# Kernel optimization log

Measured on AMD Instinct MI355X. Metric: run time of the kernel, lower is better.

The kernel has to match this reference:

```python
import jax, jax.numpy as jnp
import numpy as np

DIM = 64
OUT_DIM = 32
ALPHA = 16
BRANCH = 4
DEPTH = 7  # levels 0..DEPTH; level l has BRANCH**l nodes
SIZES = [BRANCH ** l for l in range(DEPTH + 1)]
OFFS = np.cumsum([0] + SIZES).tolist()  # OFFS[l] = start index of level l (BFS order)
N = OFFS[-1]  # 21845


def _build_children():
    # complete 4-ary tree in BFS order; leaves get 0 (never read)
    ch = np.zeros((N, BRANCH), dtype=np.int32)
    for l in range(DEPTH):
        off, size = OFFS[l], SIZES[l]
        base = OFFS[l + 1] + BRANCH * np.arange(size)
        ch[off:off + size] = base[:, None] + np.arange(BRANCH)[None, :]
    return jnp.asarray(ch)


def setup_inputs() -> dict:
    key = jax.random.key(0)
    k1, k2, k3, k4, k5 = jax.random.split(key, 5)
    sym = jax.random.randint(k1, (N,), 0, ALPHA, dtype=jnp.int32)
    children = _build_children()
    s = 1.0 / np.sqrt(DIM)
    W = jax.random.normal(k2, (ALPHA, DIM, DIM), dtype=jnp.float32) * s      # per-symbol Linear weight [out,in]
    b = jax.random.normal(k3, (ALPHA, DIM), dtype=jnp.float32) * s           # per-symbol Linear bias
    W_out = jax.random.normal(k4, (OUT_DIM, DIM), dtype=jnp.float32) * s
    b_out = jax.random.normal(k5, (OUT_DIM,), dtype=jnp.float32) * s
    return {"sym": sym, "children": children, "W": W, "b": b,
            "W_out": W_out, "b_out": b_out}


def _forward(W, b, W_out, b_out, sym, children):
    enc = jnp.zeros((N, DIM), dtype=W.dtype)
    # process levels bottom-up (children before parents) -- batches the
    # original node-by-node stack recursion by tree depth
    for l in range(DEPTH, -1, -1):
        off, size = OFFS[l], SIZES[l]
        syms = sym[off:off + size]                      # [size]
        if l == DEPTH:
            # leaves: layer applied to zero vector
            h = jnp.zeros((size, DIM), dtype=W.dtype)
        else:
            ch = children[off:off + size]               # [size, 4]
            h = enc[ch].mean(axis=1)                    # gather children encodings + mean
        Wn = W[syms]                                    # [size, dim, dim] symbol-routed weights
        bn = b[syms]                                    # [size, dim]
        e = jax.nn.sigmoid(jnp.einsum('nij,nj->ni', Wn, h) + bn)
        enc = enc.at[off:off + size].set(e)
    # root is node 0 in BFS order
    return enc[0] @ W_out.T + b_out                     # [OUT_DIM]


def reference(sym, children, W, b, W_out, b_out):
    return _forward(W, b, W_out, b_out, sym, children)
```

## Files before the change

### kernel.cpp

```cpp
#include <hip/hip_runtime.h>

#define DIM 64


__device__ __forceinline__ float sigmoidf_(float x) {
    return 1.0f / (1.0f + __expf(-x));
}

__device__ __forceinline__ float matvec_sig(const float* __restrict__ W,
                                            const float* __restrict__ B,
                                            int s, int lane,
                                            const float* h) {
    const float4* wrow = reinterpret_cast<const float4*>(W + (size_t)s * DIM * DIM + lane * DIM);
    const float4* h4   = reinterpret_cast<const float4*>(h);
    float acc = B[s * DIM + lane];
#pragma unroll
    for (int j = 0; j < DIM / 4; ++j) {
        float4 wv = wrow[j];
        float4 hv = h4[j];
        acc = fmaf(wv.x, hv.x, acc);
        acc = fmaf(wv.y, hv.y, acc);
        acc = fmaf(wv.z, hv.z, acc);
        acc = fmaf(wv.w, hv.w, acc);
    }
    return sigmoidf_(acc);
}

__global__ __launch_bounds__(256) void k_lvl654(const int* __restrict__ sym,
                                                const float* __restrict__ W,
                                                const float* __restrict__ B,
                                                float* __restrict__ enc4) {
    __shared__ __align__(16) float h6[16][DIM];
    __shared__ __align__(16) float e6[16][DIM];
    __shared__ __align__(16) float hb[4][DIM];
    __shared__ __align__(16) float e5[4][DIM];
    const int tid  = threadIdx.x;
    const int lane = tid & 63;
    const int wv   = tid >> 6;
    const int b    = blockIdx.x;

#pragma unroll
    for (int it = 0; it < 4; ++it) {
        int q = it * 4 + wv;
        int leaf0 = 5461 + b * 64 + q * 4;
        float acc = 0.0f;
#pragma unroll
        for (int c = 0; c < 4; ++c) {
            int s = sym[leaf0 + c];
            acc += sigmoidf_(B[s * DIM + lane]);
        }
        h6[q][lane] = 0.25f * acc;
    }
    __syncthreads();
#pragma unroll
    for (int it = 0; it < 4; ++it) {
        int q = it * 4 + wv;
        int p = 1365 + b * 16 + q;
        e6[q][lane] = matvec_sig(W, B, sym[p], lane, &h6[q][0]);
    }
    __syncthreads();
    hb[wv][lane] = 0.25f * (e6[4 * wv + 0][lane] + e6[4 * wv + 1][lane] +
                            e6[4 * wv + 2][lane] + e6[4 * wv + 3][lane]);
    __syncthreads();
    {
        int m = 341 + b * 4 + wv;
        e5[wv][lane] = matvec_sig(W, B, sym[m], lane, &hb[wv][0]);
    }
    __syncthreads();
    if (wv == 0) {
        hb[0][lane] = 0.25f * (e5[0][lane] + e5[1][lane] + e5[2][lane] + e5[3][lane]);
    }
    __syncthreads();
    if (wv == 0) {
        int n = 85 + b;
        enc4[b * DIM + lane] = matvec_sig(W, B, sym[n], lane, &hb[0][0]);
    }
}

__global__ __launch_bounds__(256) void k_lvl32(const int* __restrict__ sym,
                                               const float* __restrict__ W,
                                               const float* __restrict__ B,
                                               const float* __restrict__ enc4,
                                               float* __restrict__ enc2) {
    __shared__ __align__(16) float h3[4][DIM];
    __shared__ __align__(16) float e3[4][DIM];
    __shared__ __align__(16) float hb[DIM];
    const int tid  = threadIdx.x;
    const int lane = tid & 63;
    const int wv   = tid >> 6;
    const int b    = blockIdx.x;

    {
        int c0 = 16 * b + 4 * wv;
        float acc = enc4[(c0 + 0) * DIM + lane] + enc4[(c0 + 1) * DIM + lane] +
                    enc4[(c0 + 2) * DIM + lane] + enc4[(c0 + 3) * DIM + lane];
        h3[wv][lane] = 0.25f * acc;
    }
    __syncthreads();
    {
        int n = 21 + 4 * b + wv;
        e3[wv][lane] = matvec_sig(W, B, sym[n], lane, &h3[wv][0]);
    }
    __syncthreads();
    if (wv == 0) {
        hb[lane] = 0.25f * (e3[0][lane] + e3[1][lane] + e3[2][lane] + e3[3][lane]);
    }
    __syncthreads();
    if (wv == 0) {
        int n = 5 + b;
        enc2[b * DIM + lane] = matvec_sig(W, B, sym[n], lane, hb);
    }
}

__global__ __launch_bounds__(256) void k_lvl10_out(const int* __restrict__ sym,
                                                   const float* __restrict__ W,
                                                   const float* __restrict__ B,
                                                   const float* __restrict__ Wout,
                                                   const float* __restrict__ bout,
                                                   const float* __restrict__ enc2,
                                                   float* __restrict__ out) {
    __shared__ __align__(16) float h1[4][DIM];
    __shared__ __align__(16) float e1[4][DIM];
    __shared__ __align__(16) float hb[DIM];
    __shared__ __align__(16) float e0[DIM];
    const int tid  = threadIdx.x;
    const int lane = tid & 63;
    const int wv   = tid >> 6;

    {
        int c0 = 4 * wv;
        float acc = enc2[(c0 + 0) * DIM + lane] + enc2[(c0 + 1) * DIM + lane] +
                    enc2[(c0 + 2) * DIM + lane] + enc2[(c0 + 3) * DIM + lane];
        h1[wv][lane] = 0.25f * acc;
    }
    __syncthreads();
    {
        int m = 1 + wv;
        e1[wv][lane] = matvec_sig(W, B, sym[m], lane, &h1[wv][0]);
    }
    __syncthreads();
    if (wv == 0) {
        hb[lane] = 0.25f * (e1[0][lane] + e1[1][lane] + e1[2][lane] + e1[3][lane]);
    }
    __syncthreads();
    if (wv == 0) {
        e0[lane] = matvec_sig(W, B, sym[0], lane, hb);
    }
    __syncthreads();
    if (tid < 32) {
        const float4* wrow = reinterpret_cast<const float4*>(Wout + tid * DIM);
        const float4* h4   = reinterpret_cast<const float4*>(e0);
        float acc = bout[tid];
#pragma unroll
        for (int j = 0; j < DIM / 4; ++j) {
            float4 w = wrow[j];
            float4 h = h4[j];
            acc = fmaf(w.x, h.x, acc);
            acc = fmaf(w.y, h.y, acc);
            acc = fmaf(w.z, h.z, acc);
            acc = fmaf(w.w, h.w, acc);
        }
        out[tid] = acc;
    }
}

extern "C" void kernel_launch(void* const* d_in, const int* in_sizes, int n_in,
                              void* d_out, int out_size, void* d_ws, size_t ws_size,
                              hipStream_t stream) {
    const int*   sym  = (const int*)d_in[0];
    const float* W    = (const float*)d_in[2];
    const float* B    = (const float*)d_in[3];
    const float* Wout = (const float*)d_in[4];
    const float* bout = (const float*)d_in[5];
    float* out  = (float*)d_out;
    float* enc4 = (float*)d_ws;
    float* enc2 = enc4 + 256 * DIM;

    k_lvl654<<<256, 256, 0, stream>>>(sym, W, B, enc4);
    k_lvl32 <<<16,  256, 0, stream>>>(sym, W, B, enc4, enc2);
    k_lvl10_out<<<1, 256, 0, stream>>>(sym, W, B, Wout, bout, enc2, out);
}
```

Before: 83.53 us.

## Fuse three level kernels into one cooperative kernel with grid sync

```diff
diff --git a/kernel.cpp b/kernel.cpp
--- a/kernel.cpp
+++ b/kernel.cpp
@@ -1,4 +1,7 @@
 #include <hip/hip_runtime.h>
+#include <hip/hip_cooperative_groups.h>
+
+namespace cg = cooperative_groups;
 
 #define DIM 64
 
@@ -26,141 +29,109 @@
     return sigmoidf_(acc);
 }
 
-__global__ __launch_bounds__(256) void k_lvl654(const int* __restrict__ sym,
-                                                const float* __restrict__ W,
-                                                const float* __restrict__ B,
-                                                float* __restrict__ enc4) {
+__global__ __launch_bounds__(1024) void recnet_all(const int* __restrict__ sym,
+                                                   const float* __restrict__ W,
+                                                   const float* __restrict__ B,
+                                                   const float* __restrict__ Wout,
+                                                   const float* __restrict__ bout,
+                                                   float* __restrict__ enc4,
+                                                   float* __restrict__ out) {
     __shared__ __align__(16) float h6[16][DIM];
     __shared__ __align__(16) float e6[16][DIM];
+    __shared__ __align__(16) float e5[4][DIM];
     __shared__ __align__(16) float hb[4][DIM];
-    __shared__ __align__(16) float e5[4][DIM];
+    __shared__ __align__(16) float e3[64][DIM];
+    __shared__ __align__(16) float e2[16][DIM];
+
     const int tid  = threadIdx.x;
     const int lane = tid & 63;
-    const int wv   = tid >> 6;
+    const int w    = tid >> 6;
     const int b    = blockIdx.x;
 
-#pragma unroll
-    for (int it = 0; it < 4; ++it) {
-        int q = it * 4 + wv;
-        int leaf0 = 5461 + b * 64 + q * 4;
+    {
+        int leaf0 = 5461 + b * 64 + w * 4;
         float acc = 0.0f;
 #pragma unroll
         for (int c = 0; c < 4; ++c) {
             int s = sym[leaf0 + c];
             acc += sigmoidf_(B[s * DIM + lane]);
         }
-        h6[q][lane] = 0.25f * acc;
+        h6[w][lane] = 0.25f * acc;
     }
     __syncthreads();
-#pragma unroll
-    for (int it = 0; it < 4; ++it) {
-        int q = it * 4 + wv;
-        int p = 1365 + b * 16 + q;
-        e6[q][lane] = matvec_sig(W, B, sym[p], lane, &h6[q][0]);
+    {
+        int p = 1365 + b * 16 + w;
+        e6[w][lane] = matvec_sig(W, B, sym[p], lane, &h6[w][0]);
     }
     __syncthreads();
-    hb[wv][lane] = 0.25f * (e6[4 * wv + 0][lane] + e6[4 * wv + 1][lane] +
-                            e6[4 * wv + 2][lane] + e6[4 * wv + 3][lane]);
-    __syncthreads();
-    {
-        int m = 341 + b * 4 + wv;
-        e5[wv][lane] = matvec_sig(W, B, sym[m], lane, &hb[wv][0]);
+    if (w < 4) {
+        hb[w][lane] = 0.25f * (e6[4 * w + 0][lane] + e6[4 * w + 1][lane] +
+                               e6[4 * w + 2][lane] + e6[4 * w + 3][lane]);
     }
     __syncthreads();
-    if (wv == 0) {
+    if (w < 4) {
+        int m = 341 + b * 4 + w;
+        e5[w][lane] = matvec_sig(W, B, sym[m], lane, &hb[w][0]);
+    }
+    __syncthreads();
+    if (w == 0) {
         hb[0][lane] = 0.25f * (e5[0][lane] + e5[1][lane] + e5[2][lane] + e5[3][lane]);
     }
     __syncthreads();
-    if (wv == 0) {
-        int n = 85 + b;
-        enc4[b * DIM + lane] = matvec_sig(W, B, sym[n], lane, &hb[0][0]);
+    if (w == 0) {
+        enc4[b * DIM + lane] = matvec_sig(W, B, sym[85 + b], lane, &hb[0][0]);
     }
-}
 
-__global__ __launch_bounds__(256) void k_lvl32(const int* __restrict__ sym,
-                                               const float* __restrict__ W,
-                                               const float* __restrict__ B,
-                                               const float* __restrict__ enc4,
-                                               float* __restrict__ enc2) {
-    __shared__ __align__(16) float h3[4][DIM];
-    __shared__ __align__(16) float e3[4][DIM];
-    __shared__ __align__(16) float hb[DIM];
-    const int tid  = threadIdx.x;
-    const int lane = tid & 63;
-    const int wv   = tid >> 6;
-    const int b    = blockIdx.x;
+    cg::this_grid().sync();
 
-    {
-        int c0 = 16 * b + 4 * wv;
-        float acc = enc4[(c0 + 0) * DIM + lane] + enc4[(c0 + 1) * DIM + lane] +
-                    enc4[(c0 + 2) * DIM + lane] + enc4[(c0 + 3) * DIM + lane];
-        h3[wv][lane] = 0.25f * acc;
-    }
-    __syncthreads();
-    {
-        int n = 21 + 4 * b + wv;
-        e3[wv][lane] = matvec_sig(W, B, sym[n], lane, &h3[wv][0]);
-    }
-    __syncthreads();
-    if (wv == 0) {
-        hb[lane] = 0.25f * (e3[0][lane] + e3[1][lane] + e3[2][lane] + e3[3][lane]);
-    }
-    __syncthreads();
-    if (wv == 0) {
-        int n = 5 + b;
-        enc2[b * DIM + lane] = matvec_sig(W, B, sym[n], lane, hb);
-    }
-}
-
-__global__ __launch_bounds__(256) void k_lvl10_out(const int* __restrict__ sym,
-                                                   const float* __restrict__ W,
-                                                   const float* __restrict__ B,
-                                                   const float* __restrict__ Wout,
-                                                   const float* __restrict__ bout,
-                                                   const float* __restrict__ enc2,
-                                                   float* __restrict__ out) {
-    __shared__ __align__(16) float h1[4][DIM];
-    __shared__ __align__(16) float e1[4][DIM];
-    __shared__ __align__(16) float hb[DIM];
-    __shared__ __align__(16) float e0[DIM];
-    const int tid  = threadIdx.x;
-    const int lane = tid & 63;
-    const int wv   = tid >> 6;
-
-    {
-        int c0 = 4 * wv;
-        float acc = enc2[(c0 + 0) * DIM + lane] + enc2[(c0 + 1) * DIM + lane] +
-                    enc2[(c0 + 2) * DIM + lane] + enc2[(c0 + 3) * DIM + lane];
-        h1[wv][lane] = 0.25f * acc;
-    }
-    __syncthreads();
-    {
-        int m = 1 + wv;
-        e1[wv][lane] = matvec_sig(W, B, sym[m], lane, &h1[wv][0]);
-    }
-    __syncthreads();
-    if (wv == 0) {
-        hb[lane] = 0.25f * (e1[0][lane] + e1[1][lane] + e1[2][lane] + e1[3][lane]);
-    }
-    __syncthreads();
-    if (wv == 0) {
-        e0[lane] = matvec_sig(W, B, sym[0], lane, hb);
-    }
-    __syncthreads();
-    if (tid < 32) {
-        const float4* wrow = reinterpret_cast<const float4*>(Wout + tid * DIM);
-        const float4* h4   = reinterpret_cast<const float4*>(e0);
-        float acc = bout[tid];
+    if (b == 0) {
 #pragma unroll
-        for (int j = 0; j < DIM / 4; ++j) {
-            float4 w = wrow[j];
-            float4 h = h4[j];
-            acc = fmaf(w.x, h.x, acc);
-            acc = fmaf(w.y, h.y, acc);
-            acc = fmaf(w.z, h.z, acc);
-            acc = fmaf(w.w, h.w, acc);
+        for (int i = 0; i < 4; ++i) {
+            int t = w * 4 + i;
+            float hsum = enc4[(4 * t + 0) * DIM + lane] + enc4[(4 * t + 1) * DIM + lane] +
+                         enc4[(4 * t + 2) * DIM + lane] + enc4[(4 * t + 3) * DIM + lane];
+            h6[w][lane] = 0.25f * hsum;
+            __syncthreads();
+            e3[t][lane] = matvec_sig(W, B, sym[21 + t], lane, &h6[w][0]);
+            __syncthreads();
         }
-        out[tid] = acc;
+        h6[w][lane] = 0.25f * (e3[4 * w + 0][lane] + e3[4 * w + 1][lane] +
+                               e3[4 * w + 2][lane] + e3[4 * w + 3][lane]);
+        __syncthreads();
+        e2[w][lane] = matvec_sig(W, B, sym[5 + w], lane, &h6[w][0]);
+        __syncthreads();
+        if (w < 4) {
+            hb[w][lane] = 0.25f * (e2[4 * w + 0][lane] + e2[4 * w + 1][lane] +
+                                   e2[4 * w + 2][lane] + e2[4 * w + 3][lane]);
+        }
+        __syncthreads();
+        if (w < 4) {
+            e6[w][lane] = matvec_sig(W, B, sym[1 + w], lane, &hb[w][0]);
+        }
+        __syncthreads();
+        if (w == 0) {
+            hb[0][lane] = 0.25f * (e6[0][lane] + e6[1][lane] + e6[2][lane] + e6[3][lane]);
+        }
+        __syncthreads();
+        if (w == 0) {
+            h6[0][lane] = matvec_sig(W, B, sym[0], lane, &hb[0][0]);
+        }
+        __syncthreads();
+        if (tid < 32) {
+            const float4* wrow = reinterpret_cast<const float4*>(Wout + tid * DIM);
+            const float4* h4   = reinterpret_cast<const float4*>(&h6[0][0]);
+            float acc = bout[tid];
+#pragma unroll
+            for (int j = 0; j < DIM / 4; ++j) {
+                float4 wv = wrow[j];
+                float4 hv = h4[j];
+                acc = fmaf(wv.x, hv.x, acc);
+                acc = fmaf(wv.y, hv.y, acc);
+                acc = fmaf(wv.z, hv.z, acc);
+                acc = fmaf(wv.w, hv.w, acc);
+            }
+            out[tid] = acc;
+        }
     }
 }
 
@@ -174,9 +145,8 @@
     const float* bout = (const float*)d_in[5];
     float* out  = (float*)d_out;
     float* enc4 = (float*)d_ws;
-    float* enc2 = enc4 + 256 * DIM;
 
-    k_lvl654<<<256, 256, 0, stream>>>(sym, W, B, enc4);
-    k_lvl32 <<<16,  256, 0, stream>>>(sym, W, B, enc4, enc2);
-    k_lvl10_out<<<1, 256, 0, stream>>>(sym, W, B, Wout, bout, enc2, out);
+    void* args[] = {(void*)&sym, (void*)&W, (void*)&B, (void*)&Wout,
+                    (void*)&bout, (void*)&enc4, (void*)&out};
+    hipLaunchCooperativeKernel((void*)recnet_all, dim3(256), dim3(1024), args, 0, stream);
 }
```

New measurement: 152.2 us. 1.82x slower.
